# Optimization experiments

Measured on AMD Instinct MI355X. Metric: run time of the kernel, lower is better.

The kernel has to match this reference:

```python
import jax, jax.numpy as jnp
import numpy as np

N_NODES = 50000
N_EDGES = 800000
D = 64  # in_feat == hidden_channels


def _param(key, shape, fan_in):
    return jax.random.normal(key, shape, dtype=jnp.float32) / np.sqrt(fan_in)


def setup_inputs() -> dict:
    key = jax.random.key(0)
    ks = jax.random.split(key, 32)
    inp = {
        "x": jax.random.normal(ks[0], (N_NODES, D), dtype=jnp.float32),
        "edge_index": jax.random.randint(ks[1], (2, N_EDGES), 0, N_NODES, dtype=jnp.int64),
    }
    i = 2
    for l in (1, 2, 3):
        inp[f"W1_{l}"] = _param(ks[i + 0], (D, D), D)   # LEConv lin1 (source nodes)
        inp[f"b1_{l}"] = jnp.zeros((D,), jnp.float32)
        inp[f"W2_{l}"] = _param(ks[i + 1], (D, D), D)   # LEConv lin2 (target nodes, no bias)
        inp[f"W3_{l}"] = _param(ks[i + 2], (D, D), D)   # LEConv lin3 (root/self)
        inp[f"b3_{l}"] = jnp.zeros((D,), jnp.float32)
        inp[f"Wl_{l}"] = _param(ks[i + 3], (D, D), D)   # post-conv Linear
        inp[f"bl_{l}"] = jnp.zeros((D,), jnp.float32)
        i += 4
    return inp


def _leconv(x, src, dst, W1, b1, W2, W3, b3):
    # out_i = lin3(x_i) + sum_{j->i} (lin1(x_j) - lin2(x_i))
    a = x @ W1 + b1          # [N, D]
    b = x @ W2               # [N, D]
    msg = a[src] - b[dst]    # [E, D]  gather + elementwise
    agg = jax.ops.segment_sum(msg, dst, num_segments=x.shape[0])  # scatter-add
    return agg + (x @ W3 + b3)


def reference(x, edge_index,
              W1_1, b1_1, W2_1, W3_1, b3_1, Wl_1, bl_1,
              W1_2, b1_2, W2_2, W3_2, b3_2, Wl_2, bl_2,
              W1_3, b1_3, W2_3, W3_3, b3_3, Wl_3, bl_3):
    src, dst = edge_index[0], edge_index[1]
    h = x
    for (W1, b1, W2, W3, b3, Wl, bl) in (
        (W1_1, b1_1, W2_1, W3_1, b3_1, Wl_1, bl_1),
        (W1_2, b1_2, W2_2, W3_2, b3_2, Wl_2, bl_2),
        (W1_3, b1_3, W2_3, W3_3, b3_3, Wl_3, bl_3),
    ):
        h = _leconv(h, src, dst, W1, b1, W2, W3, b3)
        h = jax.nn.relu(h @ Wl + bl)
    return h
```

## Files before the change

### kernel.cpp

```cpp
#include <hip/hip_runtime.h>

#define N_NODES 50000
#define N_EDGES 800000
#define SCAN_NB ((N_NODES + 255) / 256)
#define NCHUNK 128
#define NRANGE 4
#define RNODES (N_NODES / NRANGE)
#define CEDGES (N_EDGES / NCHUNK)

typedef __attribute__((ext_vector_type(8))) short short8;
typedef __attribute__((ext_vector_type(4))) float f32x4;

struct WPtrs { const float* p[12]; };

__device__ inline unsigned short f2b(float f) {
    union { float f; unsigned u; } c; c.f = f;
    return (unsigned short)((c.u + 0x7FFFu + ((c.u >> 16) & 1u)) >> 16);
}
__device__ inline float b2f(unsigned short h) {
    union { unsigned u; float f; } c; c.u = ((unsigned)h) << 16;
    return c.f;
}

__global__ __launch_bounds__(256) void histp_kernel(const int* __restrict__ dst,
                                                    unsigned short* __restrict__ hist_part) {
    __shared__ int h[RNODES];
    const int chunk = blockIdx.x >> 2;
    const int range = blockIdx.x & 3;
    const int nbase = range * RNODES;
    for (int i = threadIdx.x; i < RNODES; i += 256) h[i] = 0;
    __syncthreads();
    const int* dp = dst + chunk * CEDGES;
    for (int i = threadIdx.x; i < CEDGES; i += 256) {
        int d = dp[i] - nbase;
        if ((unsigned)d < (unsigned)RNODES) atomicAdd(&h[d], 1);
    }
    __syncthreads();
    unsigned short* out = hist_part + (long)chunk * N_NODES + nbase;
    for (int i = threadIdx.x; i < RNODES; i += 256) out[i] = (unsigned short)h[i];
}

__global__ __launch_bounds__(256) void chunkscan_kernel(unsigned short* __restrict__ hist_part,
                                                        int* __restrict__ cnt) {
    int node = blockIdx.x * 256 + threadIdx.x;
    if (node >= N_NODES) return;
    int run = 0;
    #pragma unroll
    for (int c = 0; c < NCHUNK; ++c) {
        unsigned short* p = hist_part + (long)c * N_NODES + node;
        int v = *p;
        *p = (unsigned short)run;
        run += v;
    }
    cnt[node] = run;
}

__global__ __launch_bounds__(256) void scanA_kernel(const int* __restrict__ cnt,
                                                    int* __restrict__ off,
                                                    int* __restrict__ bsum) {
    __shared__ int tmp[256];
    const int t = threadIdx.x;
    const int i = blockIdx.x * 256 + t;
    int v = (i < N_NODES) ? cnt[i] : 0;
    tmp[t] = v;
    __syncthreads();
    #pragma unroll
    for (int d = 1; d < 256; d <<= 1) {
        int u = (t >= d) ? tmp[t - d] : 0;
        __syncthreads();
        tmp[t] += u;
        __syncthreads();
    }
    if (i < N_NODES) off[i] = tmp[t] - v;
    if (t == 255) bsum[blockIdx.x] = tmp[255];
}

__global__ __launch_bounds__(256) void scanB_kernel(const int* __restrict__ bsum,
                                                    int* __restrict__ boff,
                                                    int* __restrict__ off) {
    __shared__ int tmp[256];
    const int t = threadIdx.x;
    int v = (t < SCAN_NB) ? bsum[t] : 0;
    tmp[t] = v;
    __syncthreads();
    #pragma unroll
    for (int d = 1; d < 256; d <<= 1) {
        int u = (t >= d) ? tmp[t - d] : 0;
        __syncthreads();
        tmp[t] += u;
        __syncthreads();
    }
    if (t < SCAN_NB) boff[t] = tmp[t] - v;
    if (t == 255) off[N_NODES] = tmp[255];
}

__global__ __launch_bounds__(256) void scanC_kernel(const int* __restrict__ boff,
                                                    int* __restrict__ off) {
    int i = blockIdx.x * 256 + threadIdx.x;
    if (i < N_NODES) off[i] += boff[blockIdx.x];
}

__global__ __launch_bounds__(256) void fillp_kernel(const int* __restrict__ src,
                                                    const int* __restrict__ dst,
                                                    const int* __restrict__ off,
                                                    const unsigned short* __restrict__ hist_part,
                                                    int* __restrict__ csr) {
    __shared__ int cur[RNODES];
    const int chunk = blockIdx.x >> 2;
    const int range = blockIdx.x & 3;
    const int nbase = range * RNODES;
    const unsigned short* bp = hist_part + (long)chunk * N_NODES + nbase;
    const int* op = off + nbase;
    for (int i = threadIdx.x; i < RNODES; i += 256) cur[i] = op[i] + (int)bp[i];
    __syncthreads();
    const int* dp = dst + chunk * CEDGES;
    const int* sp = src + chunk * CEDGES;
    for (int i = threadIdx.x; i < CEDGES; i += 256) {
        int d = dp[i] - nbase;
        if ((unsigned)d < (unsigned)RNODES) {
            int pos = atomicAdd(&cur[d], 1);
            csr[pos] = sp[i];
        }
    }
}

__global__ __launch_bounds__(256) void pack_w_all_kernel(WPtrs wp,
                                                         unsigned short* __restrict__ Wp)
{
    const int layer = blockIdx.x >> 4;
    const int ct = blockIdx.x & 15;
    const float* W = wp.p[layer * 4 + (ct >> 2)];
    const int colb = (ct & 3) * 16;
    for (int local = threadIdx.x; local < 1024; local += 256) {
        int j = local & 7, lane = (local >> 3) & 63, s = local >> 9;
        int k = s * 32 + (lane >> 4) * 8 + j;
        int col = colb + (lane & 15);
        Wp[layer * 16384 + ct * 1024 + local] = f2b(W[k * 64 + col]);
    }
}

__global__ __launch_bounds__(256) void gemm3_mfma_kernel(
    const unsigned short* __restrict__ hbf, const float* __restrict__ hf32,
    const unsigned short* __restrict__ Wp,
    const float* __restrict__ b1, const float* __restrict__ b3,
    unsigned short* __restrict__ abf, unsigned short* __restrict__ bbf,
    unsigned short* __restrict__ cbf, int n)
{
    const int t = threadIdx.x;
    const int lane = t & 63;
    const int quad = lane >> 4, lm = lane & 15;
    const int row_base = blockIdx.x * 64 + (t >> 6) * 16;

    int arow = min(row_base + lm, n - 1);
    short8 a0, a1;
    if (hf32) {
        const float* hrow = hf32 + (long)arow * 64;
        #pragma unroll
        for (int j = 0; j < 8; ++j) {
            a0[j] = (short)f2b(hrow[quad * 8 + j]);
            a1[j] = (short)f2b(hrow[32 + quad * 8 + j]);
        }
    } else {
        const unsigned short* hrow = hbf + (long)arow * 64;
        a0 = *(const short8*)(hrow + quad * 8);
        a1 = *(const short8*)(hrow + 32 + quad * 8);
    }

    const short8* wp = (const short8*)Wp;
    f32x4 acc[12];
    #pragma unroll
    for (int ct = 0; ct < 12; ++ct) {
        f32x4 z = {0.f, 0.f, 0.f, 0.f};
        short8 w0 = wp[(ct * 2 + 0) * 64 + lane];
        short8 w1 = wp[(ct * 2 + 1) * 64 + lane];
        z = __builtin_amdgcn_mfma_f32_16x16x32_bf16(a0, w0, z, 0, 0, 0);
        z = __builtin_amdgcn_mfma_f32_16x16x32_bf16(a1, w1, z, 0, 0, 0);
        acc[ct] = z;
    }

    #pragma unroll
    for (int ct = 0; ct < 12; ++ct) {
        int col = ct * 16 + lm;
        float bias = 0.f;
        unsigned short* dstp;
        int lcol;
        if (ct < 4)       { bias = b1[col];        dstp = abf; lcol = col; }
        else if (ct < 8)  {                        dstp = bbf; lcol = col - 64; }
        else              { bias = b3[col - 128];  dstp = cbf; lcol = col - 128; }
        #pragma unroll
        for (int r = 0; r < 4; ++r) {
            int g = row_base + quad * 4 + r;
            if (g < n) dstp[(long)g * 64 + lcol] = f2b(acc[ct][r] + bias);
        }
    }
}

__global__ __launch_bounds__(256) void gather_kernel(
    const int* __restrict__ off, const int* __restrict__ csr,
    const unsigned short* __restrict__ abf, float* __restrict__ S, int n)
{
    int node = blockIdx.x * 4 + (threadIdx.x >> 6);
    int lane = threadIdx.x & 63;
    if (node >= n) return;
    const int g = lane >> 4;
    const int f = (lane & 15) * 4;
    int beg = off[node], end = off[node + 1];
    float ax = 0.f, ay = 0.f, az = 0.f, aw = 0.f;
    int j = beg;
    for (; j + 8 <= end; j += 8) {
        int s0 = csr[j + g], s1 = csr[j + 4 + g];
        ushort4 v0 = *(const ushort4*)(abf + (long)s0 * 64 + f);
        ushort4 v1 = *(const ushort4*)(abf + (long)s1 * 64 + f);
        ax += b2f(v0.x) + b2f(v1.x);
        ay += b2f(v0.y) + b2f(v1.y);
        az += b2f(v0.z) + b2f(v1.z);
        aw += b2f(v0.w) + b2f(v1.w);
    }
    for (; j < end; j += 4) {
        int jj = j + g;
        if (jj < end) {
            int s0 = csr[jj];
            ushort4 v0 = *(const ushort4*)(abf + (long)s0 * 64 + f);
            ax += b2f(v0.x); ay += b2f(v0.y); az += b2f(v0.z); aw += b2f(v0.w);
        }
    }
    #pragma unroll
    for (int m = 16; m < 64; m <<= 1) {
        ax += __shfl_xor(ax, m, 64);
        ay += __shfl_xor(ay, m, 64);
        az += __shfl_xor(az, m, 64);
        aw += __shfl_xor(aw, m, 64);
    }
    if (g == 0) {
        float4 o = {ax, ay, az, aw};
        *(float4*)(S + (long)node * 64 + f) = o;
    }
}

__global__ __launch_bounds__(256) void combine_mfma_kernel(
    const float* __restrict__ S, const unsigned short* __restrict__ bbf,
    const unsigned short* __restrict__ cbf, const int* __restrict__ off,
    const unsigned short* __restrict__ Wp, const float* __restrict__ bl,
    float* __restrict__ out_f, unsigned short* __restrict__ out_b,
    int n, int last)
{
    const int t = threadIdx.x;
    const int lane = t & 63;
    const int quad = lane >> 4, lm = lane & 15;
    const int row_base = blockIdx.x * 64 + (t >> 6) * 16;

    int prow = min(row_base + lm, n - 1);
    float deg = (float)(off[prow + 1] - off[prow]);

    short8 p[2];
    #pragma unroll
    for (int s = 0; s < 2; ++s) {
        int k0 = s * 32 + quad * 8;
        const float* sp = S + (long)prow * 64 + k0;
        float4 s0 = *(const float4*)sp;
        float4 s1 = *(const float4*)(sp + 4);
        const short8 bv = *(const short8*)(bbf + (long)prow * 64 + k0);
        const short8 cv = *(const short8*)(cbf + (long)prow * 64 + k0);
        float sv[8] = {s0.x, s0.y, s0.z, s0.w, s1.x, s1.y, s1.z, s1.w};
        short8 pv;
        #pragma unroll
        for (int j = 0; j < 8; ++j) {
            float v = sv[j] - deg * b2f((unsigned short)bv[j]) + b2f((unsigned short)cv[j]);
            pv[j] = (short)f2b(v);
        }
        p[s] = pv;
    }

    const short8* wp = (const short8*)Wp;
    #pragma unroll
    for (int ct = 0; ct < 4; ++ct) {
        f32x4 z = {0.f, 0.f, 0.f, 0.f};
        short8 w0 = wp[((12 + ct) * 2 + 0) * 64 + lane];
        short8 w1 = wp[((12 + ct) * 2 + 1) * 64 + lane];
        z = __builtin_amdgcn_mfma_f32_16x16x32_bf16(p[0], w0, z, 0, 0, 0);
        z = __builtin_amdgcn_mfma_f32_16x16x32_bf16(p[1], w1, z, 0, 0, 0);
        int col = ct * 16 + lm;
        float bias = bl[col];
        #pragma unroll
        for (int r = 0; r < 4; ++r) {
            int g = row_base + quad * 4 + r;
            if (g < n) {
                float v = fmaxf(z[r] + bias, 0.0f);
                if (last) out_f[(long)g * 64 + col] = v;
                else      out_b[(long)g * 64 + col] = f2b(v);
            }
        }
    }
}

extern "C" void kernel_launch(void* const* d_in, const int* in_sizes, int n_in,
                              void* d_out, int out_size, void* d_ws, size_t ws_size,
                              hipStream_t stream) {
    const float* x  = (const float*)d_in[0];
    const int*   ei = (const int*)d_in[1];
    const int*   src = ei;
    const int*   dst = ei + N_EDGES;

    char* wsb = (char*)d_ws;
    float*          S    = (float*)(wsb);
    unsigned short* hist_part = (unsigned short*)(wsb);
    unsigned short* abf  = (unsigned short*)(wsb + 12800000);
    unsigned short* bbf  = (unsigned short*)(wsb + 19200000);
    unsigned short* cbf  = (unsigned short*)(wsb + 25600000);
    unsigned short* h1   = (unsigned short*)(wsb + 32000000);
    unsigned short* Wp   = (unsigned short*)(wsb + 44800000);
    int* cnt  = (int*)(wsb + 44900000);
    int* off  = cnt + N_NODES;
    int* bsum = off + N_NODES + 1;
    int* boff = bsum + SCAN_NB;
    int* csr  = boff + SCAN_NB;

    const int NBLK = (N_NODES + 63) / 64;

    histp_kernel<<<NCHUNK * NRANGE, 256, 0, stream>>>(dst, hist_part);
    chunkscan_kernel<<<SCAN_NB, 256, 0, stream>>>(hist_part, cnt);
    scanA_kernel<<<SCAN_NB, 256, 0, stream>>>(cnt, off, bsum);
    scanB_kernel<<<1, 256, 0, stream>>>(bsum, boff, off);
    scanC_kernel<<<SCAN_NB, 256, 0, stream>>>(boff, off);
    fillp_kernel<<<NCHUNK * NRANGE, 256, 0, stream>>>(src, dst, off, hist_part, csr);

    WPtrs wps;
    for (int l = 0; l < 3; ++l) {
        int base = 2 + l * 7;
        wps.p[l * 4 + 0] = (const float*)d_in[base + 0];
        wps.p[l * 4 + 1] = (const float*)d_in[base + 2];
        wps.p[l * 4 + 2] = (const float*)d_in[base + 3];
        wps.p[l * 4 + 3] = (const float*)d_in[base + 5];
    }
    pack_w_all_kernel<<<48, 256, 0, stream>>>(wps, Wp);

    const unsigned short* hin = nullptr;
    for (int l = 0; l < 3; ++l) {
        int base = 2 + l * 7;
        const float* b1 = (const float*)d_in[base + 1];
        const float* b3 = (const float*)d_in[base + 4];
        const float* bl = (const float*)d_in[base + 6];
        const unsigned short* wp = Wp + l * 16384;

        gemm3_mfma_kernel<<<NBLK, 256, 0, stream>>>(
            hin, (l == 0) ? x : nullptr, wp, b1, b3, abf, bbf, cbf, N_NODES);

        gather_kernel<<<(N_NODES + 3) / 4, 256, 0, stream>>>(off, csr, abf, S, N_NODES);

        int last = (l == 2);
        combine_mfma_kernel<<<NBLK, 256, 0, stream>>>(
            S, bbf, cbf, off, wp, bl,
            (float*)d_out, h1, N_NODES, last);
        hin = h1;
    }
}
```

Measured before the change: 302.5 us.

## Fuse neighbor gather into combine MFMA kernel and merge chunk scan into scan

Each layer's gather now runs inside the combine kernel: each wave sums neighbor rows for 16 nodes in turn, applies the degree and self terms, stages bf16 rows in shared memory, then runs the MFMA output projection. This drops the fp32 S intermediate round trip and one launch per layer. The per-node chunk scan is folded into the first block-scan kernel to remove another launch. In exchange, the gather has far fewer waves in flight, each handling 16 nodes serially, which may reduce memory latency hiding.

```diff
diff --git a/kernel.cpp b/kernel.cpp
--- a/kernel.cpp
+++ b/kernel.cpp
@@ -40,28 +40,23 @@
     for (int i = threadIdx.x; i < RNODES; i += 256) out[i] = (unsigned short)h[i];
 }
 
-__global__ __launch_bounds__(256) void chunkscan_kernel(unsigned short* __restrict__ hist_part,
-                                                        int* __restrict__ cnt) {
-    int node = blockIdx.x * 256 + threadIdx.x;
-    if (node >= N_NODES) return;
-    int run = 0;
-    #pragma unroll
-    for (int c = 0; c < NCHUNK; ++c) {
-        unsigned short* p = hist_part + (long)c * N_NODES + node;
-        int v = *p;
-        *p = (unsigned short)run;
-        run += v;
-    }
-    cnt[node] = run;
-}
-
-__global__ __launch_bounds__(256) void scanA_kernel(const int* __restrict__ cnt,
-                                                    int* __restrict__ off,
-                                                    int* __restrict__ bsum) {
+__global__ __launch_bounds__(256) void scanA2_kernel(unsigned short* __restrict__ hist_part,
+                                                     int* __restrict__ off,
+                                                     int* __restrict__ bsum) {
     __shared__ int tmp[256];
     const int t = threadIdx.x;
-    const int i = blockIdx.x * 256 + t;
-    int v = (i < N_NODES) ? cnt[i] : 0;
+    const int node = blockIdx.x * 256 + t;
+    int run = 0;
+    if (node < N_NODES) {
+        #pragma unroll
+        for (int c = 0; c < NCHUNK; ++c) {
+            unsigned short* p = hist_part + (long)c * N_NODES + node;
+            int v = *p;
+            *p = (unsigned short)run;
+            run += v;
+        }
+    }
+    int v = run;
     tmp[t] = v;
     __syncthreads();
     #pragma unroll
@@ -71,7 +66,7 @@
         tmp[t] += u;
         __syncthreads();
     }
-    if (i < N_NODES) off[i] = tmp[t] - v;
+    if (node < N_NODES) off[node] = tmp[t] - v;
     if (t == 255) bsum[blockIdx.x] = tmp[255];
 }
 
@@ -195,81 +190,70 @@
     }
 }
 
-__global__ __launch_bounds__(256) void gather_kernel(
+__global__ __launch_bounds__(256) void gather_combine_kernel(
     const int* __restrict__ off, const int* __restrict__ csr,
-    const unsigned short* __restrict__ abf, float* __restrict__ S, int n)
-{
-    int node = blockIdx.x * 4 + (threadIdx.x >> 6);
-    int lane = threadIdx.x & 63;
-    if (node >= n) return;
-    const int g = lane >> 4;
-    const int f = (lane & 15) * 4;
-    int beg = off[node], end = off[node + 1];
-    float ax = 0.f, ay = 0.f, az = 0.f, aw = 0.f;
-    int j = beg;
-    for (; j + 8 <= end; j += 8) {
-        int s0 = csr[j + g], s1 = csr[j + 4 + g];
-        ushort4 v0 = *(const ushort4*)(abf + (long)s0 * 64 + f);
-        ushort4 v1 = *(const ushort4*)(abf + (long)s1 * 64 + f);
-        ax += b2f(v0.x) + b2f(v1.x);
-        ay += b2f(v0.y) + b2f(v1.y);
-        az += b2f(v0.z) + b2f(v1.z);
-        aw += b2f(v0.w) + b2f(v1.w);
-    }
-    for (; j < end; j += 4) {
-        int jj = j + g;
-        if (jj < end) {
-            int s0 = csr[jj];
-            ushort4 v0 = *(const ushort4*)(abf + (long)s0 * 64 + f);
-            ax += b2f(v0.x); ay += b2f(v0.y); az += b2f(v0.z); aw += b2f(v0.w);
-        }
-    }
-    #pragma unroll
-    for (int m = 16; m < 64; m <<= 1) {
-        ax += __shfl_xor(ax, m, 64);
-        ay += __shfl_xor(ay, m, 64);
-        az += __shfl_xor(az, m, 64);
-        aw += __shfl_xor(aw, m, 64);
-    }
-    if (g == 0) {
-        float4 o = {ax, ay, az, aw};
-        *(float4*)(S + (long)node * 64 + f) = o;
-    }
-}
-
-__global__ __launch_bounds__(256) void combine_mfma_kernel(
-    const float* __restrict__ S, const unsigned short* __restrict__ bbf,
-    const unsigned short* __restrict__ cbf, const int* __restrict__ off,
+    const unsigned short* __restrict__ abf,
+    const unsigned short* __restrict__ bbf,
+    const unsigned short* __restrict__ cbf,
     const unsigned short* __restrict__ Wp, const float* __restrict__ bl,
     float* __restrict__ out_f, unsigned short* __restrict__ out_b,
     int n, int last)
 {
+    __shared__ unsigned short P[64][72];
     const int t = threadIdx.x;
+    const int w = t >> 6;
     const int lane = t & 63;
-    const int quad = lane >> 4, lm = lane & 15;
-    const int row_base = blockIdx.x * 64 + (t >> 6) * 16;
-
-    int prow = min(row_base + lm, n - 1);
-    float deg = (float)(off[prow + 1] - off[prow]);
-
-    short8 p[2];
-    #pragma unroll
-    for (int s = 0; s < 2; ++s) {
-        int k0 = s * 32 + quad * 8;
-        const float* sp = S + (long)prow * 64 + k0;
-        float4 s0 = *(const float4*)sp;
-        float4 s1 = *(const float4*)(sp + 4);
-        const short8 bv = *(const short8*)(bbf + (long)prow * 64 + k0);
-        const short8 cv = *(const short8*)(cbf + (long)prow * 64 + k0);
-        float sv[8] = {s0.x, s0.y, s0.z, s0.w, s1.x, s1.y, s1.z, s1.w};
-        short8 pv;
-        #pragma unroll
-        for (int j = 0; j < 8; ++j) {
-            float v = sv[j] - deg * b2f((unsigned short)bv[j]) + b2f((unsigned short)cv[j]);
-            pv[j] = (short)f2b(v);
-        }
-        p[s] = pv;
-    }
+    const int g = lane >> 4;
+    const int f = (lane & 15) * 4;
+    const int tile0 = blockIdx.x * 64;
+    const int row_base = tile0 + w * 16;
+
+    for (int i = 0; i < 16; ++i) {
+        int nd = min(row_base + i, n - 1);
+        int beg = off[nd], end = off[nd + 1];
+        float deg = (float)(end - beg);
+        float ax = 0.f, ay = 0.f, az = 0.f, aw = 0.f;
+        int j = beg;
+        for (; j + 8 <= end; j += 8) {
+            int s0 = csr[j + g], s1 = csr[j + 4 + g];
+            ushort4 v0 = *(const ushort4*)(abf + (long)s0 * 64 + f);
+            ushort4 v1 = *(const ushort4*)(abf + (long)s1 * 64 + f);
+            ax += b2f(v0.x) + b2f(v1.x);
+            ay += b2f(v0.y) + b2f(v1.y);
+            az += b2f(v0.z) + b2f(v1.z);
+            aw += b2f(v0.w) + b2f(v1.w);
+        }
+        for (; j < end; j += 4) {
+            int jj = j + g;
+            if (jj < end) {
+                int s0 = csr[jj];
+                ushort4 v0 = *(const ushort4*)(abf + (long)s0 * 64 + f);
+                ax += b2f(v0.x); ay += b2f(v0.y); az += b2f(v0.z); aw += b2f(v0.w);
+            }
+        }
+        #pragma unroll
+        for (int m = 16; m < 64; m <<= 1) {
+            ax += __shfl_xor(ax, m, 64);
+            ay += __shfl_xor(ay, m, 64);
+            az += __shfl_xor(az, m, 64);
+            aw += __shfl_xor(aw, m, 64);
+        }
+        if (g == 0) {
+            ushort4 bv = *(const ushort4*)(bbf + (long)nd * 64 + f);
+            ushort4 cv = *(const ushort4*)(cbf + (long)nd * 64 + f);
+            ushort4 pv;
+            pv.x = f2b(ax - deg * b2f(bv.x) + b2f(cv.x));
+            pv.y = f2b(ay - deg * b2f(bv.y) + b2f(cv.y));
+            pv.z = f2b(az - deg * b2f(bv.z) + b2f(cv.z));
+            pv.w = f2b(aw - deg * b2f(bv.w) + b2f(cv.w));
+            *(ushort4*)&P[w * 16 + i][f] = pv;
+        }
+    }
+    __syncthreads();
+
+    const int quad = g, lm = lane & 15;
+    short8 p0 = *(const short8*)&P[w * 16 + lm][quad * 8];
+    short8 p1 = *(const short8*)&P[w * 16 + lm][32 + quad * 8];
 
     const short8* wp = (const short8*)Wp;
     #pragma unroll
@@ -277,17 +261,17 @@
         f32x4 z = {0.f, 0.f, 0.f, 0.f};
         short8 w0 = wp[((12 + ct) * 2 + 0) * 64 + lane];
         short8 w1 = wp[((12 + ct) * 2 + 1) * 64 + lane];
-        z = __builtin_amdgcn_mfma_f32_16x16x32_bf16(p[0], w0, z, 0, 0, 0);
-        z = __builtin_amdgcn_mfma_f32_16x16x32_bf16(p[1], w1, z, 0, 0, 0);
+        z = __builtin_amdgcn_mfma_f32_16x16x32_bf16(p0, w0, z, 0, 0, 0);
+        z = __builtin_amdgcn_mfma_f32_16x16x32_bf16(p1, w1, z, 0, 0, 0);
         int col = ct * 16 + lm;
         float bias = bl[col];
         #pragma unroll
         for (int r = 0; r < 4; ++r) {
-            int g = row_base + quad * 4 + r;
-            if (g < n) {
+            int gr = row_base + quad * 4 + r;
+            if (gr < n) {
                 float v = fmaxf(z[r] + bias, 0.0f);
-                if (last) out_f[(long)g * 64 + col] = v;
-                else      out_b[(long)g * 64 + col] = f2b(v);
+                if (last) out_f[(long)gr * 64 + col] = v;
+                else      out_b[(long)gr * 64 + col] = f2b(v);
             }
         }
     }
@@ -302,15 +286,13 @@
     const int*   dst = ei + N_EDGES;
 
     char* wsb = (char*)d_ws;
-    float*          S    = (float*)(wsb);
     unsigned short* hist_part = (unsigned short*)(wsb);
     unsigned short* abf  = (unsigned short*)(wsb + 12800000);
     unsigned short* bbf  = (unsigned short*)(wsb + 19200000);
     unsigned short* cbf  = (unsigned short*)(wsb + 25600000);
     unsigned short* h1   = (unsigned short*)(wsb + 32000000);
     unsigned short* Wp   = (unsigned short*)(wsb + 44800000);
-    int* cnt  = (int*)(wsb + 44900000);
-    int* off  = cnt + N_NODES;
+    int* off  = (int*)(wsb + 44900000);
     int* bsum = off + N_NODES + 1;
     int* boff = bsum + SCAN_NB;
     int* csr  = boff + SCAN_NB;
@@ -318,8 +300,7 @@
     const int NBLK = (N_NODES + 63) / 64;
 
     histp_kernel<<<NCHUNK * NRANGE, 256, 0, stream>>>(dst, hist_part);
-    chunkscan_kernel<<<SCAN_NB, 256, 0, stream>>>(hist_part, cnt);
-    scanA_kernel<<<SCAN_NB, 256, 0, stream>>>(cnt, off, bsum);
+    scanA2_kernel<<<SCAN_NB, 256, 0, stream>>>(hist_part, off, bsum);
     scanB_kernel<<<1, 256, 0, stream>>>(bsum, boff, off);
     scanC_kernel<<<SCAN_NB, 256, 0, stream>>>(boff, off);
     fillp_kernel<<<NCHUNK * NRANGE, 256, 0, stream>>>(src, dst, off, hist_part, csr);
@@ -345,11 +326,9 @@
         gemm3_mfma_kernel<<<NBLK, 256, 0, stream>>>(
             hin, (l == 0) ? x : nullptr, wp, b1, b3, abf, bbf, cbf, N_NODES);
 
-        gather_kernel<<<(N_NODES + 3) / 4, 256, 0, stream>>>(off, csr, abf, S, N_NODES);
-
         int last = (l == 2);
-        combine_mfma_kernel<<<NBLK, 256, 0, stream>>>(
-            S, bbf, cbf, off, wp, bl,
+        gather_combine_kernel<<<NBLK, 256, 0, stream>>>(
+            off, csr, abf, bbf, cbf, wp, bl,
             (float*)d_out, h1, N_NODES, last);
         hin = h1;
     }
```

Result: slower. 370.1 us (+22.4%).
